# Kernel tuning notes

Measured on AMD Instinct MI355X. Metric: run time of the kernel, lower is better.

Reference implementation:

```python
import jax, jax.numpy as jnp
import numpy as np

R_MAX = 10.0
NUM_BESSEL = 8
POLY_P = 5
EMB = 64
MLP_DIM = 256
NUM_LAYERS = 3
IN_DIM = 10
OUT_DIM = 1
N_NODES = 256
N_EDGES = 1024
N_GRAPHS = 16
# gated TP output: 0e channel carries 64 scalars + 128 gates (one per gated 1o/2e irrep)
GATE_MUL = {0: 3 * EMB, 1: EMB, 2: EMB}
L0_PATHS = [(0, 0, 0), (0, 1, 1), (0, 2, 2)]  # in_irreps = 64x0e
LN_PATHS = [(0, 0, 0), (1, 1, 0), (2, 2, 0), (0, 1, 1), (1, 0, 1), (1, 2, 1), (2, 1, 1), (0, 2, 2), (2, 0, 2), (1, 1, 2), (2, 2, 2)]

def _npaths(paths):
    d = {0: 0, 1: 0, 2: 0}
    for _, _, l3 in paths:
        d[l3] += 1
    return d

L0_NP = _npaths(L0_PATHS)
LN_NP = _npaths(LN_PATHS)
L0_NUMEL = sum(EMB * GATE_MUL[l3] for _, _, l3 in L0_PATHS)   # 20480
LN_NUMEL = sum(EMB * GATE_MUL[l3] for _, _, l3 in LN_PATHS)   # 69632

# ---- real spherical harmonics, component normalization (||Y_l||^2 = 2l+1) ----
def _sh_np(v):
    x, y, z = v[:, 0], v[:, 1], v[:, 2]
    s15 = np.sqrt(15.0)
    return {0: np.ones((v.shape[0], 1)),
            1: np.sqrt(3.0) * np.stack([x, y, z], 1),
            2: np.stack([s15 * x * y, s15 * y * z, 0.5 * np.sqrt(5.0) * (3 * z * z - 1), s15 * x * z, 0.5 * s15 * (x * x - y * y)], 1)}

def _rot(axis, t):
    c, s = np.cos(t), np.sin(t)
    R = np.eye(3)
    i, j = [(1, 2), (2, 0), (0, 1)][axis]
    R[i, i] = c; R[j, j] = c; R[i, j] = -s; R[j, i] = s
    return R

_PTS = np.random.RandomState(0).randn(64, 3)
_PTS /= np.linalg.norm(_PTS, axis=1, keepdims=True)

def _D(l, R):
    # rep matrix D with Y(Rv) = D @ Y(v), fit by least squares over sample points
    A = _sh_np(_PTS)[l]
    B = _sh_np(_PTS @ R.T)[l]
    return np.linalg.lstsq(A, B, rcond=None)[0].T

def _gen(l, axis, eps=1e-4):
    return (_D(l, _rot(axis, eps)) - _D(l, _rot(axis, -eps))) / (2 * eps)

def _cg(l1, l2, l3):
    # Clebsch-Gordan tensor as null space of the infinitesimal equivariance constraint
    d1, d2, d3 = 2 * l1 + 1, 2 * l2 + 1, 2 * l3 + 1
    rows = []
    for a in range(3):
        J1, J2, J3 = _gen(l1, a), _gen(l2, a), _gen(l3, a)
        rows.append(np.kron(J1.T, np.eye(d2 * d3)) + np.kron(np.eye(d1), np.kron(J2.T, np.eye(d3))) - np.kron(np.eye(d1 * d2), J3))
    _, _, Vh = np.linalg.svd(np.vstack(rows))
    c = Vh[-1].reshape(d1, d2, d3)
    c = c / np.linalg.norm(c)
    c = c * np.sign(c.flat[int(np.argmax(np.abs(c)))])
    return c

CG = {p: jnp.asarray(_cg(*p), jnp.float32) for p in set(LN_PATHS)}

def _sh_jax(u):
    x, y, z = u[..., 0], u[..., 1], u[..., 2]
    s15 = 15.0 ** 0.5
    return {0: jnp.ones_like(x)[:, None],
            1: (3.0 ** 0.5) * jnp.stack([x, y, z], -1),
            2: jnp.stack([s15 * x * y, s15 * y * z, 0.5 * (5.0 ** 0.5) * (3 * z * z - 1), s15 * x * z, 0.5 * s15 * (x * x - y * y)], -1)}

def _radial(r):
    # Bessel radial basis * polynomial cutoff envelope (MACE-style RadialEmbeddingBlock)
    n = jnp.arange(1, NUM_BESSEL + 1, dtype=r.dtype)
    bessel = (2.0 / R_MAX) ** 0.5 * jnp.sin(n * jnp.pi * r[:, None] / R_MAX) / r[:, None]
    x = r / R_MAX
    p = POLY_P
    env = 1.0 - 0.5 * (p + 1) * (p + 2) * x ** p + p * (p + 2) * x ** (p + 1) - 0.5 * p * (p + 1) * x ** (p + 2)
    env = env * (x < 1.0)
    return bessel * env[:, None]

def _conv(h, sh, ef, recv, send, paths, n_per, w1, b1, w2, b2):
    # TensorProductConvLayer: MLP(edge_feats) -> TP weights, CG tensor product, scatter-sum, gate
    E = ef.shape[0]
    w = jax.nn.relu(ef @ w1 + b1) @ w2 + b2  # (E, weight_numel)
    msgs = {0: 0.0, 1: 0.0, 2: 0.0}
    off = 0
    for (l1, l2, l3) in paths:
        mv = GATE_MUL[l3]
        wp = w[:, off:off + EMB * mv].reshape(E, EMB, mv)
        off += EMB * mv
        tmp = jnp.einsum('eui,ej,ijk->euk', h[l1][send], sh[l2], CG[(l1, l2, l3)])
        alpha = float(1.0 / np.sqrt(EMB * n_per[l3]))  # fan-in path normalization
        msgs[l3] = msgs[l3] + alpha * jnp.einsum('euk,euv->evk', tmp, wp)
    agg = {l: jax.ops.segment_sum(msgs[l], recv, num_segments=N_NODES) for l in msgs}
    s = agg[0][..., 0]  # (N, 192): 64 scalars + 128 gates
    return {0: jax.nn.silu(s[:, :EMB])[:, :, None],
            1: agg[1] * jax.nn.sigmoid(s[:, EMB:2 * EMB])[:, :, None],
            2: agg[2] * jax.nn.sigmoid(s[:, 2 * EMB:])[:, :, None]}

def _forward(atoms, pos, edge_index, batch, emb, l0_fc1_w, l0_fc1_b, l0_fc2_w, l0_fc2_b, fcs1_w, fcs1_b, fcs2_w, fcs2_b, pred_w1, pred_b1, pred_w2, pred_b2):
    recv, send = edge_index[0], edge_index[1]
    vec = pos[recv] - pos[send]
    r = jnp.maximum(jnp.linalg.norm(vec, axis=-1), 1e-6)
    sh = _sh_jax(vec / r[:, None])
    ef = _radial(r)
    h = {0: emb[atoms][:, :, None]}  # (N, 64, 1) scalar features
    h_new = _conv(h, sh, ef, recv, send, L0_PATHS, L0_NP, l0_fc1_w, l0_fc1_b, l0_fc2_w, l0_fc2_b)
    h_new[0] = h_new[0] + h[0]  # residual; F.pad means only scalar block overlaps
    h = h_new
    for i in range(NUM_LAYERS - 1):
        h_new = _conv(h, sh, ef, recv, send, LN_PATHS, LN_NP, fcs1_w[i], fcs1_b[i], fcs2_w[i], fcs2_b[i])
        h = {l: h_new[l] + h[l] for l in h_new}
    pooled = jax.ops.segment_sum(h[0][..., 0], batch, num_segments=N_GRAPHS)  # out[:, :emb_dim]
    return jax.nn.relu(pooled @ pred_w1 + pred_b1) @ pred_w2 + pred_b2

def setup_inputs():
    key = jax.random.key(0)
    ks = jax.random.split(key, 12)
    def lin(k, fi, fo):
        return jax.random.normal(k, (fi, fo), jnp.float32) * float(1.0 / np.sqrt(fi))
    return dict(
        atoms=jax.random.randint(ks[0], (N_NODES,), 0, IN_DIM),
        pos=jax.random.normal(ks[1], (N_NODES, 3), jnp.float32) * 2.0,
        edge_index=jax.random.randint(ks[2], (2, N_EDGES), 0, N_NODES),
        batch=jnp.sort(jax.random.randint(ks[3], (N_NODES,), 0, N_GRAPHS)),
        emb=jax.random.normal(ks[4], (IN_DIM, EMB), jnp.float32),
        l0_fc1_w=lin(ks[5], NUM_BESSEL, MLP_DIM), l0_fc1_b=jnp.zeros((MLP_DIM,), jnp.float32),
        l0_fc2_w=lin(ks[6], MLP_DIM, L0_NUMEL), l0_fc2_b=jnp.zeros((L0_NUMEL,), jnp.float32),
        fcs1_w=jax.random.normal(ks[7], (NUM_LAYERS - 1, NUM_BESSEL, MLP_DIM), jnp.float32) * float(1.0 / np.sqrt(NUM_BESSEL)),
        fcs1_b=jnp.zeros((NUM_LAYERS - 1, MLP_DIM), jnp.float32),
        fcs2_w=jax.random.normal(ks[8], (NUM_LAYERS - 1, MLP_DIM, LN_NUMEL), jnp.float32) * float(1.0 / np.sqrt(MLP_DIM)),
        fcs2_b=jnp.zeros((NUM_LAYERS - 1, LN_NUMEL), jnp.float32),
        pred_w1=lin(ks[9], EMB, EMB), pred_b1=jnp.zeros((EMB,), jnp.float32),
        pred_w2=lin(ks[10], EMB, OUT_DIM), pred_b2=jnp.zeros((OUT_DIM,), jnp.float32),
    )

def reference(atoms, pos, edge_index, batch, emb, l0_fc1_w, l0_fc1_b, l0_fc2_w, l0_fc2_b, fcs1_w, fcs1_b, fcs2_w, fcs2_b, pred_w1, pred_b1, pred_w2, pred_b2):
    return _forward(atoms, pos, edge_index, batch, emb, l0_fc1_w, l0_fc1_b, l0_fc2_w, l0_fc2_b, fcs1_w, fcs1_b, fcs2_w, fcs2_b, pred_w1, pred_b1, pred_w2, pred_b2)
```

## Files before the change

### kernel.cpp

```cpp
#include <hip/hip_runtime.h>
#include <hip/hip_bf16.h>
#include <math.h>

#define NE 1024
#define NN 256
#define NG 16
#define EMB 64
#define KD 256
#define BK 64
#define NUMEL_L0 20480
#define NUMEL_LN 69632
#define MSGW 704
#define MAXE 256

typedef __attribute__((ext_vector_type(8))) __bf16 bf16x8;
typedef __attribute__((ext_vector_type(4))) float f32x4;
typedef __attribute__((ext_vector_type(4))) unsigned int u32x4;

__device__ __align__(16) float g_sh[NE * 8];
__device__ __align__(16) float g_ef[NE * 8];
__device__ __align__(16) unsigned short g_hidb[NE * KD];
__device__ __align__(16) unsigned short g_w2t[(size_t)NUMEL_LN * KD];
__device__ __align__(16) unsigned short g_wb[(size_t)NE * NUMEL_LN];
__device__ __align__(16) float g_msgs[NE * MSGW];
__device__ __align__(16) float g_h0[NN * EMB];
__device__ __align__(16) float g_h1[NN * EMB * 3];
__device__ __align__(16) float g_h2[NN * EMB * 5];
__device__ int g_elist[NN * MAXE];
__device__ int g_ecnt[NN];
__device__ float g_cg[363];

__device__ __forceinline__ unsigned short f2b(float x) {
    __hip_bfloat16 h = __float2bfloat16(x);
    return *(unsigned short*)&h;
}
__device__ __forceinline__ float b2f(unsigned short u) {
    __hip_bfloat16 h;
    *(unsigned short*)&h = u;
    return __bfloat162float(h);
}

__device__ __forceinline__ void gld16(const void* g, void* l) {
    __builtin_amdgcn_global_load_lds(
        (const __attribute__((address_space(1))) unsigned int*)g,
        (__attribute__((address_space(3))) unsigned int*)l, 16, 0, 0);
}

struct Path { int l1, l2, d1, d2, d3, mv, off, cgoff, tmpoff; };

__constant__ Path PLN[11] = {
    {0, 0, 1, 1, 1, 192, 0,     0,   0},
    {1, 1, 3, 3, 1, 192, 12288, 1,   64},
    {2, 2, 5, 5, 1, 192, 24576, 10,  128},
    {0, 1, 1, 3, 3, 64,  36864, 35,  192},
    {1, 0, 3, 1, 3, 64,  40960, 44,  384},
    {1, 2, 3, 5, 3, 64,  45056, 53,  576},
    {2, 1, 5, 3, 3, 64,  49152, 98,  768},
    {0, 2, 1, 5, 5, 64,  53248, 143, 960},
    {2, 0, 5, 1, 5, 64,  57344, 168, 1280},
    {1, 1, 3, 3, 5, 64,  61440, 193, 1600},
    {2, 2, 5, 5, 5, 64,  65536, 238, 1920},
};
__constant__ Path PL0[3] = {
    {0, 0, 1, 1, 1, 192, 0,     0,   0},
    {0, 1, 1, 3, 3, 64,  12288, 35,  64},
    {0, 2, 1, 5, 5, 64,  16384, 143, 256},
};

__device__ void init_cg_body() {
    for (int i = 0; i < 363; i++) g_cg[i] = 0.f;
    const float K3 = 0.57735026918962576f;
    const float K5 = 0.44721359549995794f;
    const float A  = 0.31622776601683794f;
    const float B  = 0.18257418583505536f;
    const float C2 = 0.36514837167011072f;
    const float P  = 0.23904572186687872f;
    const float Q  = 0.20701966780270626f;
    const float S  = 0.11952286093343936f;
    g_cg[0] = 1.f;
    for (int i = 0; i < 3; i++) g_cg[1 + i * 3 + i] = K3;
    for (int i = 0; i < 5; i++) g_cg[10 + i * 5 + i] = K5;
    for (int i = 0; i < 3; i++) g_cg[35 + i * 3 + i] = K3;
    for (int i = 0; i < 3; i++) g_cg[44 + i * 3 + i] = K3;
    g_cg[53 + 1]  = A;  g_cg[53 + 15] = A;  g_cg[53 + 20] = A;
    g_cg[53 + 34] = A;  g_cg[53 + 11] = A;  g_cg[53 + 39] = A;
    g_cg[53 + 6]  = -B; g_cg[53 + 22] = -B; g_cg[53 + 38] = C2;
    g_cg[53 + 12] = A;  g_cg[53 + 28] = -A;
    g_cg[98 + 1]  = A;  g_cg[98 + 3]  = A;  g_cg[98 + 14] = A;
    g_cg[98 + 16] = A;  g_cg[98 + 29] = A;  g_cg[98 + 33] = A;
    g_cg[98 + 18] = -B; g_cg[98 + 22] = -B; g_cg[98 + 26] = C2;
    g_cg[98 + 36] = A;  g_cg[98 + 40] = -A;
    for (int i = 0; i < 5; i++) g_cg[143 + i * 5 + i] = K5;
    for (int i = 0; i < 5; i++) g_cg[168 + i * 5 + i] = K5;
    g_cg[193 + 5]  = A;  g_cg[193 + 15] = A;  g_cg[193 + 26] = A;
    g_cg[193 + 36] = A;  g_cg[193 + 13] = A;  g_cg[193 + 33] = A;
    g_cg[193 + 2]  = -B; g_cg[193 + 22] = -B; g_cg[193 + 42] = C2;
    g_cg[193 + 4]  = A;  g_cg[193 + 24] = -A;
    g_cg[238 + 2]   = P;  g_cg[238 + 10]  = P;  g_cg[238 + 50]  = P;
    g_cg[238 + 8]   = -Q; g_cg[238 + 16]  = -Q; g_cg[238 + 28]  = -Q;
    g_cg[238 + 40]  = -Q; g_cg[238 + 76]  = -Q; g_cg[238 + 80]  = -Q;
    g_cg[238 + 32]  = -S; g_cg[238 + 36]  = -S; g_cg[238 + 56]  = -S;
    g_cg[238 + 34]  = Q;  g_cg[238 + 46]  = Q;  g_cg[238 + 106] = Q;
    g_cg[238 + 62]  = -P;
    g_cg[238 + 74]  = P;  g_cg[238 + 114] = P;  g_cg[238 + 122] = P;
    g_cg[238 + 68]  = -S; g_cg[238 + 88]  = -S; g_cg[238 + 92]  = -S;
    g_cg[238 + 94]  = -Q; g_cg[238 + 98]  = -Q; g_cg[238 + 118] = -Q;
}

__global__ __launch_bounds__(256) void k_setup(const int* ei, const float* pos,
                                               const int* atoms, const float* emb) {
    int bid = blockIdx.x, tid = threadIdx.x;
    if (bid == 0) {
        if (tid == 0) init_cg_body();
        return;
    }
    if (bid <= 4) {
        int e = (bid - 1) * 256 + tid;
        int recv = ei[e], send = ei[NE + e];
        float vx = pos[recv * 3 + 0] - pos[send * 3 + 0];
        float vy = pos[recv * 3 + 1] - pos[send * 3 + 1];
        float vz = pos[recv * 3 + 2] - pos[send * 3 + 2];
        float rn = sqrtf(vx * vx + vy * vy + vz * vz);
        float r = fmaxf(rn, 1e-6f);
        float x = vx / r, y = vy / r, z = vz / r;
        const float S3 = 1.7320508075688772f;
        const float S15 = 3.8729833462074170f;
        const float S5H = 1.1180339887498949f;
        const float S15H = 1.9364916731037085f;
        g_sh[e * 8 + 0] = S3 * x;
        g_sh[e * 8 + 1] = S3 * y;
        g_sh[e * 8 + 2] = S3 * z;
        g_sh[e * 8 + 3] = S15 * x * y;
        g_sh[e * 8 + 4] = S15 * y * z;
        g_sh[e * 8 + 5] = S5H * (3.f * z * z - 1.f);
        g_sh[e * 8 + 6] = S15 * x * z;
        g_sh[e * 8 + 7] = S15H * (x * x - y * y);
        float xr = r * 0.1f;
        float env = 0.f;
        if (xr < 1.f) {
            float x5 = xr * xr * xr * xr * xr;
            env = 1.f - 21.f * x5 + 35.f * x5 * xr - 15.f * x5 * xr * xr;
        }
        const float SB = 0.44721359549995794f;
        const float PI = 3.14159265358979323846f;
        for (int nb = 1; nb <= 8; nb++) {
            g_ef[e * 8 + nb - 1] = SB * sinf((float)nb * PI * r * 0.1f) / r * env;
        }
        return;
    }
    if (bid <= 68) {
        int idx = (bid - 5) * 256 + tid;
        int n = idx / EMB, u = idx % EMB;
        g_h0[idx] = emb[atoms[n] * EMB + u];
        for (int k = 0; k < 3; k++) g_h1[idx * 3 + k] = 0.f;
        for (int k = 0; k < 5; k++) g_h2[idx * 5 + k] = 0.f;
        return;
    }
    {
        int n = bid - 69;
        int lane = tid & 63, w = tid >> 6;
        __shared__ int wsum[4];
        int mask = 0;
#pragma unroll
        for (int i = 0; i < 4; i++) {
            if (ei[tid * 4 + i] == n) mask |= 1 << i;
        }
        int nm = __popc(mask);
        int incl = nm;
#pragma unroll
        for (int off = 1; off < 64; off <<= 1) {
            int v = __shfl_up(incl, off);
            if (lane >= off) incl += v;
        }
        if (lane == 63) wsum[w] = incl;
        __syncthreads();
        int wbase = 0;
        for (int i = 0; i < w; i++) wbase += wsum[i];
        int base = wbase + incl - nm;
#pragma unroll
        for (int i = 0; i < 4; i++) {
            if (mask & (1 << i)) g_elist[n * MAXE + base++] = tid * 4 + i;
        }
        if (tid == 255) g_ecnt[n] = wbase + incl;
    }
}

__global__ __launch_bounds__(256) void k_w2t_hid(const float* w2, int numel,
                                                 const float* w1, const float* b1) {
    __shared__ float t[32][33];
    int bid = blockIdx.x;
    int nw2 = (numel >> 5) << 3;
    if (bid < nw2) {
        int n0 = (bid >> 3) * 32, k0 = (bid & 7) * 32;
        int tx = threadIdx.x & 31, ty = threadIdx.x >> 5;
#pragma unroll
        for (int i = 0; i < 4; i++) {
            int kl = ty * 4 + i;
            t[kl][tx] = w2[(size_t)(k0 + kl) * numel + n0 + tx];
        }
        __syncthreads();
#pragma unroll
        for (int i = 0; i < 4; i++) {
            int nl = ty * 4 + i;
            g_w2t[(size_t)(n0 + nl) * KD + k0 + tx] = f2b(t[tx][nl]);
        }
    } else {
        int e = bid - nw2, m = threadIdx.x;
        float acc = b1[m];
        for (int nb = 0; nb < 8; nb++) acc += g_ef[e * 8 + nb] * w1[nb * KD + m];
        g_hidb[e * KD + m] = f2b(fmaxf(acc, 0.f));
    }
}

__global__ __launch_bounds__(256) void k_gemm_mfma(const float* b2, int numel) {
    __shared__ unsigned short S[16384];
    int tid = threadIdx.x;
    int lane = tid & 63, wid = tid >> 6;
    int wm = wid >> 1, wn = wid & 1;
    int id = blockIdx.x;
    int xcd = id & 7;
    int q = id >> 3;
    int mb = q & 7;
    int ytile = q >> 3;
    int nt = xcd + 8 * ytile;
    int m0 = mb * 128, n0 = nt * 128;
    int fr = lane & 15;
    int ko = (lane >> 4) * 8;

    const char* gA = (const char*)g_hidb;
    const char* gB = (const char*)g_w2t;
    f32x4 acc[4][4] = {};

    for (int kst = 0; kst < 4; kst++) {
#pragma unroll
        for (int i = 0; i < 4; i++) {
            int L = wid * 4096 + i * 1024 + lane * 16;
            int row = L >> 7, p = L & 127;
            int sp = p ^ ((row & 7) << 4);
            gld16(gA + ((size_t)(m0 + row) * KD + kst * BK) * 2 + sp, (char*)S + L);
        }
#pragma unroll
        for (int i = 0; i < 4; i++) {
            int L = wid * 4096 + i * 1024 + lane * 16;
            int row = L >> 7, p = L & 127;
            int sp = p ^ ((row & 7) << 4);
            gld16(gB + ((size_t)(n0 + row) * KD + kst * BK) * 2 + sp, (char*)S + 16384 + L);
        }
        __syncthreads();
#pragma unroll
        for (int ks = 0; ks < 2; ks++) {
            int klb = ks * 64 + ko * 2;
            bf16x8 af[4], bf_[4];
#pragma unroll
            for (int f = 0; f < 4; f++) {
                int ra = wm * 64 + f * 16 + fr;
                af[f] = *(bf16x8*)((char*)S + ra * 128 + (klb ^ ((ra & 7) << 4)));
                int rb = wn * 64 + f * 16 + fr;
                bf_[f] = *(bf16x8*)((char*)S + 16384 + rb * 128 + (klb ^ ((rb & 7) << 4)));
            }
#pragma unroll
            for (int i = 0; i < 4; i++)
#pragma unroll
                for (int j = 0; j < 4; j++)
                    acc[i][j] = __builtin_amdgcn_mfma_f32_16x16x32_bf16(af[i], bf_[j], acc[i][j], 0, 0, 0);
        }
        __syncthreads();
    }

#pragma unroll
    for (int j = 0; j < 4; j++) {
        int colL = wn * 64 + j * 16 + fr;
        float bb = b2[n0 + colL];
#pragma unroll
        for (int i = 0; i < 4; i++) {
#pragma unroll
            for (int r = 0; r < 4; r++) {
                int rowL = wm * 64 + i * 16 + (lane >> 4) * 4 + r;
                *(unsigned short*)((char*)S + rowL * 256 + ((colL * 2) ^ ((rowL & 7) << 4))) =
                    f2b(acc[i][j][r] + bb);
            }
        }
    }
    __syncthreads();
    for (int c = tid; c < 2048; c += 256) {
        int row = c >> 4, p16 = (c & 15) * 16;
        u32x4 v = *(u32x4*)((char*)S + row * 256 + (p16 ^ ((row & 7) << 4)));
        *(u32x4*)((char*)(g_wb + (size_t)(m0 + row) * numel + n0) + p16) = v;
    }
}

__global__ __launch_bounds__(256) void k_contract(const int* ei, int numel, int layer0) {
    int e = blockIdx.x;
    int tid = threadIdx.x;
    __shared__ float tmp[2240];
    __shared__ __align__(16) unsigned short wlds[64 * 192];
    const Path* PT = layer0 ? PL0 : PLN;
    int npaths = layer0 ? 3 : 11;
    int tmptot = layer0 ? 576 : 2240;
    const unsigned short* wrow = g_wb + (size_t)e * numel;

    {
        Path pp = PT[0];
        int cnt16 = (64 * pp.mv) >> 3;
        const char* src = (const char*)(wrow + pp.off);
        for (int c = tid; c < cnt16; c += 256)
            gld16(src + c * 16, (char*)wlds + c * 16);
    }

    int send = ei[NE + e];
    for (int t = tid; t < tmptot; t += 256) {
        int p = npaths - 1;
        while (t < PT[p].tmpoff) p--;
        Path pp = PT[p];
        int rem = t - pp.tmpoff;
        int u = rem / pp.d3, k = rem % pp.d3;
        float acc = 0.f;
        for (int i = 0; i < pp.d1; i++) {
            float hv = (pp.l1 == 0) ? g_h0[send * EMB + u]
                     : (pp.l1 == 1) ? g_h1[(send * EMB + u) * 3 + i]
                                    : g_h2[(send * EMB + u) * 5 + i];
            for (int j = 0; j < pp.d2; j++) {
                float sv = (pp.l2 == 0) ? 1.f
                         : (pp.l2 == 1 ? g_sh[e * 8 + j] : g_sh[e * 8 + 3 + j]);
                acc += hv * sv * g_cg[pp.cgoff + (i * pp.d2 + j) * pp.d3 + k];
            }
        }
        tmp[t] = acc;
    }
    __syncthreads();

    float alpha0 = layer0 ? 0.125f : 0.07216878364870323f;
    float alpha12 = layer0 ? 0.125f : 0.0625f;
    int g0 = layer0 ? 1 : 3, g1 = layer0 ? 2 : 7;
    int v3 = tid / 3, k3 = tid - v3 * 3;
    int v5a = tid / 5, k5a = tid - v5a * 5;
    int p5b = 256 + tid;
    int v5b = p5b / 5, k5b = p5b - v5b * 5;
    float a0 = 0.f, a1 = 0.f;

    for (int p = 0; p < npaths; p++) {
        Path pp = PT[p];
        if (p == 0 || p == g0 || p == g1) { a0 = 0.f; a1 = 0.f; }
        int to = pp.tmpoff;
        if (pp.d3 == 1) {
            if (tid < 192) {
                for (int u = 0; u < 64; u++)
                    a0 += tmp[to + u] * b2f(wlds[u * 192 + tid]);
            }
        } else if (pp.d3 == 3) {
            if (tid < 192) {
                for (int u = 0; u < 64; u++)
                    a0 += tmp[to + u * 3 + k3] * b2f(wlds[u * 64 + v3]);
            }
        } else {
            for (int u = 0; u < 64; u++)
                a0 += tmp[to + u * 5 + k5a] * b2f(wlds[u * 64 + v5a]);
            if (tid < 64) {
                for (int u = 0; u < 64; u++)
                    a1 += tmp[to + u * 5 + k5b] * b2f(wlds[u * 64 + v5b]);
            }
        }
        if (p == g0 - 1 && tid < 192) g_msgs[e * MSGW + tid] = alpha0 * a0;
        if (p == g1 - 1 && tid < 192) g_msgs[e * MSGW + 192 + tid] = alpha12 * a0;
        if (p == npaths - 1) {
            g_msgs[e * MSGW + 384 + tid] = alpha12 * a0;
            if (tid < 64) g_msgs[e * MSGW + 640 + tid] = alpha12 * a1;
        }
        __syncthreads();
        if (p + 1 < npaths) {
            Path pn = PT[p + 1];
            int cnt16 = (64 * pn.mv) >> 3;
            const char* src = (const char*)(wrow + pn.off);
            for (int c = tid; c < cnt16; c += 256)
                gld16(src + c * 16, (char*)wlds + c * 16);
            __syncthreads();
        }
    }
}

__global__ __launch_bounds__(256) void k_agggate() {
    int n = blockIdx.x, tid = threadIdx.x;
    __shared__ float agg[MSGW];
    int cnt = g_ecnt[n];
    for (int d = tid; d < MSGW; d += 256) {
        float a = 0.f;
        for (int idx = 0; idx < cnt; idx++) {
            int e = g_elist[n * MAXE + idx];
            a += g_msgs[e * MSGW + d];
        }
        agg[d] = a;
    }
    __syncthreads();
    if (tid < EMB) {
        int u = tid;
        float s0 = agg[u], s1 = agg[64 + u], s2 = agg[128 + u];
        float sg0 = 1.f / (1.f + expf(-s0));
        float g0 = s0 * sg0;
        float sg1 = 1.f / (1.f + expf(-s1));
        float sg2 = 1.f / (1.f + expf(-s2));
        g_h0[n * EMB + u] += g0;
        for (int k = 0; k < 3; k++) g_h1[(n * EMB + u) * 3 + k] += agg[192 + u * 3 + k] * sg1;
        for (int k = 0; k < 5; k++) g_h2[(n * EMB + u) * 5 + k] += agg[384 + u * 5 + k] * sg2;
    }
}

__global__ __launch_bounds__(1024) void k_poolhead(const int* batch, const float* w1,
                                                   const float* b1, const float* w2,
                                                   const float* b2, float* out) {
    __shared__ float pl[NG * EMB];
    int g = threadIdx.x >> 6, u = threadIdx.x & 63;
    float a = 0.f;
    for (int n = 0; n < NN; n++)
        if (batch[n] == g) a += g_h0[n * EMB + u];
    pl[g * EMB + u] = a;
    __syncthreads();
    float t = b1[u];
    for (int uu = 0; uu < EMB; uu++) t += pl[g * EMB + uu] * w1[uu * EMB + u];
    t = fmaxf(t, 0.f);
    float contrib = t * w2[u];
    for (int off = 32; off > 0; off >>= 1) contrib += __shfl_down(contrib, off);
    if (u == 0) out[g] = contrib + b2[0];
}

extern "C" void kernel_launch(void* const* d_in, const int* in_sizes, int n_in,
                              void* d_out, int out_size, void* d_ws, size_t ws_size,
                              hipStream_t stream) {
    const int* atoms = (const int*)d_in[0];
    const float* pos = (const float*)d_in[1];
    const int* ei = (const int*)d_in[2];
    const int* batch = (const int*)d_in[3];
    const float* emb = (const float*)d_in[4];
    const float* l0w1 = (const float*)d_in[5];
    const float* l0b1 = (const float*)d_in[6];
    const float* l0w2 = (const float*)d_in[7];
    const float* l0b2 = (const float*)d_in[8];
    const float* f1w = (const float*)d_in[9];
    const float* f1b = (const float*)d_in[10];
    const float* f2w = (const float*)d_in[11];
    const float* f2b = (const float*)d_in[12];
    const float* pw1 = (const float*)d_in[13];
    const float* pb1 = (const float*)d_in[14];
    const float* pw2 = (const float*)d_in[15];
    const float* pb2 = (const float*)d_in[16];
    float* out = (float*)d_out;

    k_setup<<<dim3(325), dim3(256), 0, stream>>>(ei, pos, atoms, emb);

    for (int layer = 0; layer < 3; layer++) {
        const float* w1 = layer == 0 ? l0w1 : f1w + (size_t)(layer - 1) * 8 * KD;
        const float* b1 = layer == 0 ? l0b1 : f1b + (size_t)(layer - 1) * KD;
        const float* w2 = layer == 0 ? l0w2 : f2w + (size_t)(layer - 1) * KD * NUMEL_LN;
        const float* b2 = layer == 0 ? l0b2 : f2b + (size_t)(layer - 1) * NUMEL_LN;
        int numel = layer == 0 ? NUMEL_L0 : NUMEL_LN;
        int layer0 = layer == 0 ? 1 : 0;
        k_w2t_hid<<<dim3((numel / 32) * 8 + NE), dim3(256), 0, stream>>>(w2, numel, w1, b1);
        k_gemm_mfma<<<dim3((numel / 128) * (NE / 128)), dim3(256), 0, stream>>>(b2, numel);
        k_contract<<<dim3(NE), dim3(256), 0, stream>>>(ei, numel, layer0);
        k_agggate<<<dim3(NN), dim3(256), 0, stream>>>();
    }

    k_poolhead<<<dim3(1), dim3(1024), 0, stream>>>(batch, pw1, pb1, pw2, pb2, out);
}
```

Baseline: 523.2 us.

## Split contraction per edge into three output-group blocks and read weights directly

The per-edge contraction kernel now launches three blocks per edge, one for each output irrep group (0e, 1o, 2e). Each block computes only its slice of the intermediate tensor and reduces over its own paths. The shared-memory weight staging and per-path barriers are removed; bf16 weights are read straight from global memory in unrolled loops. This raises block-level parallelism and removes synchronisation, at the cost of uncoalesced global weight reads and some redundant input loads per block.

```diff
diff --git a/kernel.cpp b/kernel.cpp
--- a/kernel.cpp
+++ b/kernel.cpp
@@ -291,28 +291,25 @@
 
 __global__ __launch_bounds__(256) void k_contract(const int* ei, int numel, int layer0) {
     int e = blockIdx.x;
+    int grp = blockIdx.y;
     int tid = threadIdx.x;
-    __shared__ float tmp[2240];
-    __shared__ __align__(16) unsigned short wlds[64 * 192];
+    __shared__ float tmp[1280];
     const Path* PT = layer0 ? PL0 : PLN;
     int npaths = layer0 ? 3 : 11;
-    int tmptot = layer0 ? 576 : 2240;
+    int pstart = layer0 ? grp : (grp == 0 ? 0 : (grp == 1 ? 3 : 7));
+    int pend   = layer0 ? grp + 1 : (grp == 0 ? 3 : (grp == 1 ? 7 : 11));
+    int tbase = PT[pstart].tmpoff;
+    int tend  = (pend < npaths) ? PT[pend].tmpoff : (layer0 ? 576 : 2240);
+    int ttot = tend - tbase;
     const unsigned short* wrow = g_wb + (size_t)e * numel;
-
-    {
-        Path pp = PT[0];
-        int cnt16 = (64 * pp.mv) >> 3;
-        const char* src = (const char*)(wrow + pp.off);
-        for (int c = tid; c < cnt16; c += 256)
-            gld16(src + c * 16, (char*)wlds + c * 16);
-    }
-
     int send = ei[NE + e];
-    for (int t = tid; t < tmptot; t += 256) {
-        int p = npaths - 1;
-        while (t < PT[p].tmpoff) p--;
+
+    for (int t = tid; t < ttot; t += 256) {
+        int tt = t + tbase;
+        int p = pend - 1;
+        while (tt < PT[p].tmpoff) p--;
         Path pp = PT[p];
-        int rem = t - pp.tmpoff;
+        int rem = tt - pp.tmpoff;
         int u = rem / pp.d3, k = rem % pp.d3;
         float acc = 0.f;
         for (int i = 0; i < pp.d1; i++) {
@@ -331,50 +328,46 @@
 
     float alpha0 = layer0 ? 0.125f : 0.07216878364870323f;
     float alpha12 = layer0 ? 0.125f : 0.0625f;
-    int g0 = layer0 ? 1 : 3, g1 = layer0 ? 2 : 7;
     int v3 = tid / 3, k3 = tid - v3 * 3;
     int v5a = tid / 5, k5a = tid - v5a * 5;
     int p5b = 256 + tid;
     int v5b = p5b / 5, k5b = p5b - v5b * 5;
     float a0 = 0.f, a1 = 0.f;
 
-    for (int p = 0; p < npaths; p++) {
+    for (int p = pstart; p < pend; p++) {
         Path pp = PT[p];
-        if (p == 0 || p == g0 || p == g1) { a0 = 0.f; a1 = 0.f; }
-        int to = pp.tmpoff;
+        int to = pp.tmpoff - tbase;
+        const unsigned short* wp = wrow + pp.off;
         if (pp.d3 == 1) {
             if (tid < 192) {
+#pragma unroll 16
                 for (int u = 0; u < 64; u++)
-                    a0 += tmp[to + u] * b2f(wlds[u * 192 + tid]);
+                    a0 += tmp[to + u] * b2f(wp[u * 192 + tid]);
             }
         } else if (pp.d3 == 3) {
             if (tid < 192) {
+#pragma unroll 16
                 for (int u = 0; u < 64; u++)
-                    a0 += tmp[to + u * 3 + k3] * b2f(wlds[u * 64 + v3]);
+                    a0 += tmp[to + u * 3 + k3] * b2f(wp[u * 64 + v3]);
             }
         } else {
+#pragma unroll 16
             for (int u = 0; u < 64; u++)
-                a0 += tmp[to + u * 5 + k5a] * b2f(wlds[u * 64 + v5a]);
+                a0 += tmp[to + u * 5 + k5a] * b2f(wp[u * 64 + v5a]);
             if (tid < 64) {
+#pragma unroll 16
                 for (int u = 0; u < 64; u++)
-                    a1 += tmp[to + u * 5 + k5b] * b2f(wlds[u * 64 + v5b]);
-            }
-        }
-        if (p == g0 - 1 && tid < 192) g_msgs[e * MSGW + tid] = alpha0 * a0;
-        if (p == g1 - 1 && tid < 192) g_msgs[e * MSGW + 192 + tid] = alpha12 * a0;
-        if (p == npaths - 1) {
-            g_msgs[e * MSGW + 384 + tid] = alpha12 * a0;
-            if (tid < 64) g_msgs[e * MSGW + 640 + tid] = alpha12 * a1;
-        }
-        __syncthreads();
-        if (p + 1 < npaths) {
-            Path pn = PT[p + 1];
-            int cnt16 = (64 * pn.mv) >> 3;
-            const char* src = (const char*)(wrow + pn.off);
-            for (int c = tid; c < cnt16; c += 256)
-                gld16(src + c * 16, (char*)wlds + c * 16);
-            __syncthreads();
-        }
+                    a1 += tmp[to + u * 5 + k5b] * b2f(wp[u * 64 + v5b]);
+            }
+        }
+    }
+    if (grp == 0) {
+        if (tid < 192) g_msgs[e * MSGW + tid] = alpha0 * a0;
+    } else if (grp == 1) {
+        if (tid < 192) g_msgs[e * MSGW + 192 + tid] = alpha12 * a0;
+    } else {
+        g_msgs[e * MSGW + 384 + tid] = alpha12 * a0;
+        if (tid < 64) g_msgs[e * MSGW + 640 + tid] = alpha12 * a1;
     }
 }
 
@@ -455,7 +448,7 @@
         int layer0 = layer == 0 ? 1 : 0;
         k_w2t_hid<<<dim3((numel / 32) * 8 + NE), dim3(256), 0, stream>>>(w2, numel, w1, b1);
         k_gemm_mfma<<<dim3((numel / 128) * (NE / 128)), dim3(256), 0, stream>>>(b2, numel);
-        k_contract<<<dim3(NE), dim3(256), 0, stream>>>(ei, numel, layer0);
+        k_contract<<<dim3(NE, 3), dim3(256), 0, stream>>>(ei, numel, layer0);
         k_agggate<<<dim3(NN), dim3(256), 0, stream>>>();
     }
 
```

Result: faster. 424.2 us (-18.9%).
